# Optimization experiments

Measured on AMD Instinct MI355X. Metric: run time of the kernel, lower is better.

## Reference

```python
import jax, jax.numpy as jnp
import numpy as np

D_MODEL = 2048
N_HEADS = 32
N_KV_HEADS = 8
HEAD_DIM = D_MODEL // N_HEADS  # 64
ROPE_THETA = 10000.0


def _build_rope_cache(seq_len, head_dim, theta):
    half = head_dim // 2
    inv_freq = 1.0 / theta ** (jnp.arange(half, dtype=jnp.float32) / half)
    pos = jnp.arange(seq_len, dtype=jnp.float32)
    freqs = jnp.outer(pos, inv_freq)  # [S, half]
    return jnp.cos(freqs), jnp.sin(freqs)


def _apply_rope(x, cos, sin):
    # x: [B, H, S, D]; cos/sin: [S, D//2] -> broadcast [1,1,S,D//2]
    x_even = x[..., ::2]
    x_odd = x[..., 1::2]
    c = cos[None, None]
    s = sin[None, None]
    rot_even = x_even * c - x_odd * s
    rot_odd = x_even * s + x_odd * c
    # interleave back: stack on last axis then flatten
    return jnp.stack((rot_even, rot_odd), axis=-1).reshape(x.shape)


def setup_inputs() -> dict:
    key = jax.random.key(0)
    k0, k1, k2, k3, k4 = jax.random.split(key, 5)
    B, S = 2, 2048
    scale = 0.02
    x = jax.random.normal(k0, (B, S, D_MODEL), dtype=jnp.float32)
    Wq = jax.random.normal(k1, (D_MODEL, N_HEADS * HEAD_DIM), dtype=jnp.float32) * scale
    Wk = jax.random.normal(k2, (D_MODEL, N_KV_HEADS * HEAD_DIM), dtype=jnp.float32) * scale
    Wv = jax.random.normal(k3, (D_MODEL, N_KV_HEADS * HEAD_DIM), dtype=jnp.float32) * scale
    Wo = jax.random.normal(k4, (D_MODEL, D_MODEL), dtype=jnp.float32) * scale
    return {"x": x, "Wq": Wq, "Wk": Wk, "Wv": Wv, "Wo": Wo}


def reference(x, Wq, Wk, Wv, Wo):
    B, S, _ = x.shape
    q = (x @ Wq).reshape(B, S, N_HEADS, HEAD_DIM).transpose(0, 2, 1, 3)      # [B,H,S,D]
    k = (x @ Wk).reshape(B, S, N_KV_HEADS, HEAD_DIM).transpose(0, 2, 1, 3)   # [B,Hk,S,D]
    v = (x @ Wv).reshape(B, S, N_KV_HEADS, HEAD_DIM).transpose(0, 2, 1, 3)
    cos, sin = _build_rope_cache(S, HEAD_DIM, ROPE_THETA)
    q = _apply_rope(q, cos, sin)
    k = _apply_rope(k, cos, sin)
    repeat = N_HEADS // N_KV_HEADS
    if repeat > 1:
        k = jnp.repeat(k, repeat, axis=1)
        v = jnp.repeat(v, repeat, axis=1)
    scores = jnp.einsum("bhqd,bhkd->bhqk", q, k) / jnp.sqrt(jnp.float32(HEAD_DIM))
    causal = jnp.tril(jnp.ones((S, S), dtype=bool))
    neg = -jnp.finfo(scores.dtype).max
    scores = jnp.where(causal[None, None], scores, neg)
    probs = jax.nn.softmax(scores.astype(jnp.float32), axis=-1).astype(x.dtype)
    out = jnp.einsum("bhqk,bhkd->bhqd", probs, v)
    out = out.transpose(0, 2, 1, 3).reshape(B, S, D_MODEL)
    return out @ Wo
```

## Files before the change

kernel.cpp:

```cpp
#include <hip/hip_runtime.h>
#include <cstdint>

typedef unsigned short u16;
typedef __attribute__((ext_vector_type(8))) __bf16 bf16x8;
typedef __attribute__((ext_vector_type(4))) float f32x4;

#define S_LEN 2048

__device__ __forceinline__ u16 f2bf(float f) {
  uint32_t u = __builtin_bit_cast(uint32_t, f);
  u += 0x7fffu + ((u >> 16) & 1u);
  return (u16)(u >> 16);
}
__device__ __forceinline__ float bf2f(u16 h) {
  return __builtin_bit_cast(float, (uint32_t)h << 16);
}
__device__ __forceinline__ bf16x8 ldfrag(const u16* p) {
  return __builtin_bit_cast(bf16x8, *(const uint4*)p);
}
__device__ __forceinline__ f32x4 mfma16(bf16x8 a, bf16x8 b, f32x4 c) {
  return __builtin_amdgcn_mfma_f32_16x16x32_bf16(a, b, c, 0, 0, 0);
}
__device__ __forceinline__ void glds16(const u16* g, u16* l) {
  __builtin_amdgcn_global_load_lds((const __attribute__((address_space(1))) void*)g,
                                   (__attribute__((address_space(3))) void*)l, 16, 0, 0);
}

__global__ __launch_bounds__(256) void cvt_kernel(const float* __restrict__ in,
                                                  u16* __restrict__ out, int n4) {
  int i = blockIdx.x * 256 + threadIdx.x;
  if (i >= n4) return;
  float4 v = ((const float4*)in)[i];
  ushort4 o;
  o.x = f2bf(v.x); o.y = f2bf(v.y); o.z = f2bf(v.z); o.w = f2bf(v.w);
  ((ushort4*)out)[i] = o;
}

__global__ __launch_bounds__(256) void cvtT_kernel(const float* __restrict__ W,
                                                   u16* __restrict__ Wt, int K, int N) {
  __shared__ float t[32][33];
  int tx = threadIdx.x & 31, ty = threadIdx.x >> 5;
  int n0 = blockIdx.x * 32, k0 = blockIdx.y * 32;
#pragma unroll
  for (int j = 0; j < 4; ++j)
    t[ty + 8 * j][tx] = W[(long)(k0 + ty + 8 * j) * N + n0 + tx];
  __syncthreads();
#pragma unroll
  for (int j = 0; j < 4; ++j)
    Wt[(long)(n0 + ty + 8 * j) * K + k0 + tx] = f2bf(t[tx][ty + 8 * j]);
}

template <int MODE>
__global__ __launch_bounds__(256) void gemm_bt(const u16* __restrict__ A,
                                               const u16* __restrict__ Bt,
                                               void* __restrict__ C, int K, int ldc,
                                               u16* __restrict__ Kc_out,
                                               u16* __restrict__ Vt_out) {
  __shared__ __align__(16) u16 As[3][4096];
  __shared__ __align__(16) u16 Bs[3][4096];
  int tid = threadIdx.x;
  int lane = tid & 63, w = tid >> 6;
  int wr = (w >> 1) * 64, wc = (w & 1) * 64;
  int l15 = lane & 15, l4 = lane >> 4;
  int rowbase = blockIdx.x * 128, colbase = blockIdx.y * 128;
  f32x4 acc[4][4] = {};
  int r0 = tid >> 2, kc0 = (tid & 3) * 8;
  const u16* Ap0 = A + (long)(rowbase + r0) * K + kc0;
  const u16* Ap1 = A + (long)(rowbase + 64 + r0) * K + kc0;
  const u16* Bp0 = Bt + (long)(colbase + r0) * K + kc0;
  const u16* Bp1 = Bt + (long)(colbase + 64 + r0) * K + kc0;
  int wb = w * 512;
  auto stage = [&](int t, int buf) {
    int ko = t * 32;
    glds16(Ap0 + ko, &As[buf][wb]);
    glds16(Ap1 + ko, &As[buf][2048 + wb]);
    glds16(Bp0 + ko, &Bs[buf][wb]);
    glds16(Bp1 + ko, &Bs[buf][2048 + wb]);
  };
  int nk = K >> 5;
  stage(0, 0);
  stage(1, 1);
  asm volatile("s_waitcnt vmcnt(4)" ::: "memory");
  __builtin_amdgcn_s_barrier();
  int cur = 0, nxt2 = 2;
  for (int t = 0; t < nk; ++t) {
    if (t + 2 < nk) stage(t + 2, nxt2);
    bf16x8 af[4], bv[4];
#pragma unroll
    for (int m = 0; m < 4; ++m) af[m] = ldfrag(&As[cur][(wr + m * 16 + l15) * 32 + l4 * 8]);
#pragma unroll
    for (int n = 0; n < 4; ++n) bv[n] = ldfrag(&Bs[cur][(wc + n * 16 + l15) * 32 + l4 * 8]);
#pragma unroll
    for (int m = 0; m < 4; ++m)
#pragma unroll
      for (int n = 0; n < 4; ++n) acc[m][n] = mfma16(af[m], bv[n], acc[m][n]);
    if (t + 1 < nk) {
      if (t + 2 < nk)
        asm volatile("s_waitcnt vmcnt(4)" ::: "memory");
      else
        asm volatile("s_waitcnt vmcnt(0)" ::: "memory");
      __builtin_amdgcn_s_barrier();
    }
    cur = cur == 2 ? 0 : cur + 1;
    nxt2 = nxt2 == 2 ? 0 : nxt2 + 1;
  }
  if (MODE == 0) {
#pragma unroll
    for (int m = 0; m < 4; ++m)
#pragma unroll
      for (int n = 0; n < 4; ++n)
#pragma unroll
        for (int r = 0; r < 4; ++r) {
          int row = rowbase + wr + m * 16 + l4 * 4 + r;
          int col = colbase + wc + n * 16 + l15;
          ((float*)C)[(long)row * ldc + col] = acc[m][n][r];
        }
  } else {
    if (colbase < 2048) {
#pragma unroll
      for (int m = 0; m < 4; ++m)
#pragma unroll
        for (int n = 0; n < 4; ++n)
#pragma unroll
          for (int r = 0; r < 4; ++r) {
            int row = rowbase + wr + m * 16 + l4 * 4 + r;
            int col = colbase + wc + n * 16 + l15;
            ((u16*)C)[(long)row * 2048 + col] = f2bf(acc[m][n][r]);
          }
    } else if (colbase < 2560) {
#pragma unroll
      for (int m = 0; m < 4; ++m)
#pragma unroll
        for (int n = 0; n < 4; ++n)
#pragma unroll
          for (int r = 0; r < 4; ++r) {
            int row = rowbase + wr + m * 16 + l4 * 4 + r;
            int col = colbase + wc + n * 16 + l15 - 2048;
            Kc_out[(long)row * 512 + col] = f2bf(acc[m][n][r]);
          }
    } else {
#pragma unroll
      for (int m = 0; m < 4; ++m)
#pragma unroll
        for (int n = 0; n < 4; ++n) {
          int row = rowbase + wr + m * 16 + l4 * 4;
          int col = colbase + wc + n * 16 + l15 - 2560;
          int b_ = row >> 11, s_ = row & 2047;
          int kvh_ = col >> 6, d_ = col & 63;
          ushort4 pk;
          pk.x = f2bf(acc[m][n][0]); pk.y = f2bf(acc[m][n][1]);
          pk.z = f2bf(acc[m][n][2]); pk.w = f2bf(acc[m][n][3]);
          *(ushort4*)&Vt_out[((long)((b_ * 8 + kvh_) * 64 + d_)) * 2048 + s_] = pk;
        }
    }
  }
}

__global__ __launch_bounds__(256) void rope_tab_kernel(float2* __restrict__ ctab) {
  int idx = blockIdx.x * 256 + threadIdx.x;
  int i = idx & 31, s = idx >> 5;
  float freq = exp2f(-(float)i * (13.287712379549449f / 32.0f));
  float sn, cs;
  sincosf((float)s * freq, &sn, &cs);
  ctab[idx] = make_float2(cs, sn);
}

__global__ __launch_bounds__(256) void kpack_kernel(const u16* __restrict__ Ks,
                                                    const float2* __restrict__ ctab,
                                                    u16* __restrict__ Kp) {
  int idx = blockIdx.x * 256 + threadIdx.x;
  int lane = idx & 63, half = (idx >> 6) & 1, n = (idx >> 7) & 3;
  int t = (idx >> 9) & 31, kvh = (idx >> 14) & 7, b = idx >> 17;
  int l15 = lane & 15, l4 = lane >> 4;
  int s = t * 64 + n * 16 + l15;
  int d0 = half * 32 + l4 * 8;
  const u16* src = Ks + ((long)(b * 2048 + s)) * 512 + kvh * 64 + d0;
  uint4 v = *(const uint4*)src;
  const float2* ct = ctab + s * 32 + (d0 >> 1);
  uint32_t o[4];
#pragma unroll
  for (int jj = 0; jj < 4; ++jj) {
    uint32_t vw = ((const uint32_t*)&v)[jj];
    float2 cs = ct[jj];
    float e = bf2f((u16)vw), od = bf2f((u16)(vw >> 16));
    float re = e * cs.x - od * cs.y;
    float ro = e * cs.y + od * cs.x;
    o[jj] = (uint32_t)f2bf(re) | ((uint32_t)f2bf(ro) << 16);
  }
  *(uint4*)(Kp + (long)idx * 8) = *(uint4*)o;
}

__global__ __launch_bounds__(256) void vpack_kernel(const u16* __restrict__ Vt,
                                                    u16* __restrict__ Vp) {
  int idx = blockIdx.x * 256 + threadIdx.x;
  int lane = idx & 63, half = (idx >> 6) & 1, f = (idx >> 7) & 3;
  int t = (idx >> 9) & 31, kvh = (idx >> 14) & 7, b = idx >> 17;
  int l15 = lane & 15, l4 = lane >> 4;
  const u16* src = Vt + ((long)((b * 8 + kvh) * 64 + f * 16 + l15)) * 2048 +
                   t * 64 + half * 32 + l4 * 8;
  *(uint4*)(Vp + (long)idx * 8) = *(const uint4*)src;
}

__global__ __launch_bounds__(256, 8) void attn_kernel(const u16* __restrict__ Q,
                                                      const u16* __restrict__ Kp,
                                                      const u16* __restrict__ Vp,
                                                      const float2* __restrict__ ctab,
                                                      u16* __restrict__ O) {
  int bid = blockIdx.x;
  int p = bid & 31, h = (bid >> 5) & 31, b = bid >> 10;
  int kvh = h >> 2;
  int tid = threadIdx.x, lane = tid & 63, w = tid >> 6;
  int l15 = lane & 15, l4 = lane >> 4;
  int cc = (w + p) & 3;
  int c = cc == 0 ? 2 * p : cc == 1 ? 2 * p + 1 : cc == 2 ? 127 - 2 * p : 126 - 2 * p;
  int qb = c * 16;
  int nt = (c >> 2) + 1;
  __shared__ u16 Ps[4][16][72];
  u16(*myPs)[72] = Ps[w];
  const u16* Qh = Q + (long)b * S_LEN * 2048 + h * 64;
  const u16* Kh = Kp + (long)(b * 8 + kvh) * 131072;
  const u16* Vh = Vp + (long)(b * 8 + kvh) * 131072;
  u16* Oh = O + (long)b * S_LEN * 2048 + h * 64;
  int s = qb + l15;
  const u16* qp = Qh + (long)s * 2048;
  uint4 r0 = *(const uint4*)(qp + l4 * 8);
  uint4 r1 = *(const uint4*)(qp + 32 + l4 * 8);
  const float2* ct = ctab + (long)s * 32 + l4 * 4;
  uint32_t q0w[4], q1w[4];
#pragma unroll
  for (int jj = 0; jj < 4; ++jj) {
    float2 cs0 = ct[jj], cs1 = ct[16 + jj];
    uint32_t v0 = ((const uint32_t*)&r0)[jj], v1 = ((const uint32_t*)&r1)[jj];
    float e0 = bf2f((u16)v0), o0 = bf2f((u16)(v0 >> 16));
    float e1 = bf2f((u16)v1), o1 = bf2f((u16)(v1 >> 16));
    float a0 = (e0 * cs0.x - o0 * cs0.y) * 0.125f;
    float b0 = (e0 * cs0.y + o0 * cs0.x) * 0.125f;
    float a1 = (e1 * cs1.x - o1 * cs1.y) * 0.125f;
    float b1 = (e1 * cs1.y + o1 * cs1.x) * 0.125f;
    q0w[jj] = (uint32_t)f2bf(a0) | ((uint32_t)f2bf(b0) << 16);
    q1w[jj] = (uint32_t)f2bf(a1) | ((uint32_t)f2bf(b1) << 16);
  }
  bf16x8 qf0 = __builtin_bit_cast(bf16x8, *(uint4*)q0w);
  bf16x8 qf1 = __builtin_bit_cast(bf16x8, *(uint4*)q1w);
  float m_r = -INFINITY, l_r = 0.f;
  f32x4 oaccT[4] = {};
  int lane8 = lane * 8;
  for (int t = 0; t < nt; ++t) {
    const u16* kt = Kh + t * 4096;
    f32x4 sacc[4] = {};
#pragma unroll
    for (int n = 0; n < 4; ++n) {
      sacc[n] = mfma16(ldfrag(kt + n * 1024 + lane8), qf0, sacc[n]);
      sacc[n] = mfma16(ldfrag(kt + n * 1024 + 512 + lane8), qf1, sacc[n]);
    }
    if (t == nt - 1) {
      int kb = t * 64;
#pragma unroll
      for (int n = 0; n < 4; ++n) {
        int kc_ = kb + n * 16 + l4 * 4;
#pragma unroll
        for (int r = 0; r < 4; ++r)
          if (kc_ + r > qb + l15) sacc[n][r] = -1e30f;
      }
    }
    float mx = fmaxf(fmaxf(fmaxf(sacc[0][0], sacc[0][1]), fmaxf(sacc[0][2], sacc[0][3])),
                     fmaxf(fmaxf(sacc[1][0], sacc[1][1]), fmaxf(sacc[1][2], sacc[1][3])));
    mx = fmaxf(mx, fmaxf(fmaxf(fmaxf(sacc[2][0], sacc[2][1]), fmaxf(sacc[2][2], sacc[2][3])),
                         fmaxf(fmaxf(sacc[3][0], sacc[3][1]), fmaxf(sacc[3][2], sacc[3][3]))));
    mx = fmaxf(mx, __shfl_xor(mx, 16));
    mx = fmaxf(mx, __shfl_xor(mx, 32));
    float mn = fmaxf(m_r, mx);
    float fac = __expf(m_r - mn);
    m_r = mn;
    float rs = 0.f;
#pragma unroll
    for (int n = 0; n < 4; ++n) {
      float p0 = __expf(sacc[n][0] - mn);
      float p1 = __expf(sacc[n][1] - mn);
      float p2 = __expf(sacc[n][2] - mn);
      float p3 = __expf(sacc[n][3] - mn);
      rs += (p0 + p1) + (p2 + p3);
      ushort4 pk;
      pk.x = f2bf(p0); pk.y = f2bf(p1); pk.z = f2bf(p2); pk.w = f2bf(p3);
      *(ushort4*)&myPs[l15][n * 16 + l4 * 4] = pk;
    }
    rs += __shfl_xor(rs, 16);
    rs += __shfl_xor(rs, 32);
    l_r = l_r * fac + rs;
#pragma unroll
    for (int f = 0; f < 4; ++f) {
      oaccT[f][0] *= fac; oaccT[f][1] *= fac;
      oaccT[f][2] *= fac; oaccT[f][3] *= fac;
    }
    bf16x8 pa0 = ldfrag(&myPs[l15][l4 * 8]);
    bf16x8 pa1 = ldfrag(&myPs[l15][32 + l4 * 8]);
    const u16* vt = Vh + t * 4096;
#pragma unroll
    for (int f = 0; f < 4; ++f) {
      oaccT[f] = mfma16(ldfrag(vt + f * 1024 + lane8), pa0, oaccT[f]);
      oaccT[f] = mfma16(ldfrag(vt + f * 1024 + 512 + lane8), pa1, oaccT[f]);
    }
  }
  float linv = 1.f / l_r;
#pragma unroll
  for (int f = 0; f < 4; ++f) {
    ushort4 pk;
    pk.x = f2bf(oaccT[f][0] * linv); pk.y = f2bf(oaccT[f][1] * linv);
    pk.z = f2bf(oaccT[f][2] * linv); pk.w = f2bf(oaccT[f][3] * linv);
    *(ushort4*)&Oh[(long)(qb + l15) * 2048 + f * 16 + l4 * 4] = pk;
  }
}

extern "C" void kernel_launch(void* const* d_in, const int* in_sizes, int n_in,
                              void* d_out, int out_size, void* d_ws, size_t ws_size,
                              hipStream_t stream) {
  const float* x = (const float*)d_in[0];
  const float* Wq = (const float*)d_in[1];
  const float* Wk = (const float*)d_in[2];
  const float* Wv = (const float*)d_in[3];
  const float* Wo = (const float*)d_in[4];
  float* out = (float*)d_out;
  char* ws = (char*)d_ws;
  u16* xb = (u16*)(ws + 0);
  u16* WqkvT = (u16*)(ws + 16777216);
  u16* WoT = (u16*)(ws + 29360128);
  u16* Qs = (u16*)(ws + 37748736);
  u16* Ks = (u16*)(ws + 54525952);
  u16* Vt = (u16*)(ws + 58720256);
  u16* Os = (u16*)(ws + 62914560);
  u16* Kp = (u16*)(ws + 0);
  u16* Vp = (u16*)(ws + 4194304);
  float2* ctab = (float2*)(ws + 79691776);

  cvt_kernel<<<8192, 256, 0, stream>>>(x, xb, 2097152);
  cvtT_kernel<<<dim3(64, 64), 256, 0, stream>>>(Wq, WqkvT, 2048, 2048);
  cvtT_kernel<<<dim3(16, 64), 256, 0, stream>>>(Wk, WqkvT + 4194304, 2048, 512);
  cvtT_kernel<<<dim3(16, 64), 256, 0, stream>>>(Wv, WqkvT + 5242880, 2048, 512);
  cvtT_kernel<<<dim3(64, 64), 256, 0, stream>>>(Wo, WoT, 2048, 2048);
  rope_tab_kernel<<<256, 256, 0, stream>>>(ctab);
  gemm_bt<3><<<dim3(32, 24), 256, 0, stream>>>(xb, WqkvT, Qs, 2048, 2048, Ks, Vt);
  kpack_kernel<<<1024, 256, 0, stream>>>(Ks, ctab, Kp);
  vpack_kernel<<<1024, 256, 0, stream>>>(Vt, Vp);
  attn_kernel<<<2048, 256, 0, stream>>>(Qs, Kp, Vp, ctab, Os);
  gemm_bt<0><<<dim3(32, 16), 256, 0, stream>>>(Os, WoT, out, 2048, 2048, nullptr, nullptr);
}
```

Baseline: 369.3 us.

## Merge prep and pack launches, use exp2 softmax, hardware bf16 cvt, setprio

Merges the six conversion/rope-table launches into one prep kernel and the K/V pack kernels into one, cutting launch overhead and gaps between kernels. The f32-to-bf16 conversion now uses the hardware cast. Softmax switches to exp2 with log2(e) folded into the Q scale. MFMA sections are wrapped in s_setprio, and attention query-block assignment changes from a balanced interleave to a simple linear mapping. The simpler mapping may worsen load balance across causal blocks.

```diff
diff --git a/kernel.cpp b/kernel.cpp
--- a/kernel.cpp
+++ b/kernel.cpp
@@ -8,9 +8,11 @@
 #define S_LEN 2048
 
 __device__ __forceinline__ u16 f2bf(float f) {
-  uint32_t u = __builtin_bit_cast(uint32_t, f);
-  u += 0x7fffu + ((u >> 16) & 1u);
-  return (u16)(u >> 16);
+  __bf16 h = (__bf16)f;
+  return __builtin_bit_cast(u16, h);
+}
+__device__ __forceinline__ uint32_t pk2(float a, float b) {
+  return (uint32_t)f2bf(a) | ((uint32_t)f2bf(b) << 16);
 }
 __device__ __forceinline__ float bf2f(u16 h) {
   return __builtin_bit_cast(float, (uint32_t)h << 16);
@@ -26,21 +28,10 @@
                                    (__attribute__((address_space(3))) void*)l, 16, 0, 0);
 }
 
-__global__ __launch_bounds__(256) void cvt_kernel(const float* __restrict__ in,
-                                                  u16* __restrict__ out, int n4) {
-  int i = blockIdx.x * 256 + threadIdx.x;
-  if (i >= n4) return;
-  float4 v = ((const float4*)in)[i];
-  ushort4 o;
-  o.x = f2bf(v.x); o.y = f2bf(v.y); o.z = f2bf(v.z); o.w = f2bf(v.w);
-  ((ushort4*)out)[i] = o;
-}
-
-__global__ __launch_bounds__(256) void cvtT_kernel(const float* __restrict__ W,
-                                                   u16* __restrict__ Wt, int K, int N) {
-  __shared__ float t[32][33];
-  int tx = threadIdx.x & 31, ty = threadIdx.x >> 5;
-  int n0 = blockIdx.x * 32, k0 = blockIdx.y * 32;
+__device__ __forceinline__ void cvtT_body(const float* __restrict__ W, u16* __restrict__ Wt,
+                                          int K, int N, int n0, int k0, int tid,
+                                          float (*t)[33]) {
+  int tx = tid & 31, ty = tid >> 5;
 #pragma unroll
   for (int j = 0; j < 4; ++j)
     t[ty + 8 * j][tx] = W[(long)(k0 + ty + 8 * j) * N + n0 + tx];
@@ -48,6 +39,46 @@
 #pragma unroll
   for (int j = 0; j < 4; ++j)
     Wt[(long)(n0 + ty + 8 * j) * K + k0 + tx] = f2bf(t[tx][ty + 8 * j]);
+}
+
+__global__ __launch_bounds__(256) void prep_kernel(const float* __restrict__ x,
+                                                   const float* __restrict__ Wq,
+                                                   const float* __restrict__ Wk,
+                                                   const float* __restrict__ Wv,
+                                                   const float* __restrict__ Wo,
+                                                   u16* __restrict__ xb,
+                                                   u16* __restrict__ WqkvT,
+                                                   u16* __restrict__ WoT,
+                                                   float2* __restrict__ ctab) {
+  __shared__ float t[32][33];
+  int blk = blockIdx.x, tid = threadIdx.x;
+  if (blk < 8192) {
+    int i = blk * 256 + tid;
+    float4 v = ((const float4*)x)[i];
+    uint2 o;
+    o.x = pk2(v.x, v.y);
+    o.y = pk2(v.z, v.w);
+    ((uint2*)xb)[i] = o;
+  } else if (blk < 12288) {
+    int b2 = blk - 8192;
+    cvtT_body(Wq, WqkvT, 2048, 2048, (b2 & 63) * 32, (b2 >> 6) * 32, tid, t);
+  } else if (blk < 13312) {
+    int b2 = blk - 12288;
+    cvtT_body(Wk, WqkvT + 4194304, 2048, 512, (b2 & 15) * 32, (b2 >> 4) * 32, tid, t);
+  } else if (blk < 14336) {
+    int b2 = blk - 13312;
+    cvtT_body(Wv, WqkvT + 5242880, 2048, 512, (b2 & 15) * 32, (b2 >> 4) * 32, tid, t);
+  } else if (blk < 18432) {
+    int b2 = blk - 14336;
+    cvtT_body(Wo, WoT, 2048, 2048, (b2 & 63) * 32, (b2 >> 6) * 32, tid, t);
+  } else {
+    int idx = (blk - 18432) * 256 + tid;
+    int i = idx & 31, s = idx >> 5;
+    float freq = exp2f(-(float)i * (13.287712379549449f / 32.0f));
+    float sn, cs;
+    sincosf((float)s * freq, &sn, &cs);
+    ctab[idx] = make_float2(cs, sn);
+  }
 }
 
 template <int MODE>
@@ -147,58 +178,49 @@
           int col = colbase + wc + n * 16 + l15 - 2560;
           int b_ = row >> 11, s_ = row & 2047;
           int kvh_ = col >> 6, d_ = col & 63;
-          ushort4 pk;
-          pk.x = f2bf(acc[m][n][0]); pk.y = f2bf(acc[m][n][1]);
-          pk.z = f2bf(acc[m][n][2]); pk.w = f2bf(acc[m][n][3]);
-          *(ushort4*)&Vt_out[((long)((b_ * 8 + kvh_) * 64 + d_)) * 2048 + s_] = pk;
+          uint2 o2;
+          o2.x = pk2(acc[m][n][0], acc[m][n][1]);
+          o2.y = pk2(acc[m][n][2], acc[m][n][3]);
+          *(uint2*)&Vt_out[((long)((b_ * 8 + kvh_) * 64 + d_)) * 2048 + s_] = o2;
         }
     }
   }
 }
 
-__global__ __launch_bounds__(256) void rope_tab_kernel(float2* __restrict__ ctab) {
-  int idx = blockIdx.x * 256 + threadIdx.x;
-  int i = idx & 31, s = idx >> 5;
-  float freq = exp2f(-(float)i * (13.287712379549449f / 32.0f));
-  float sn, cs;
-  sincosf((float)s * freq, &sn, &cs);
-  ctab[idx] = make_float2(cs, sn);
-}
-
-__global__ __launch_bounds__(256) void kpack_kernel(const u16* __restrict__ Ks,
-                                                    const float2* __restrict__ ctab,
-                                                    u16* __restrict__ Kp) {
-  int idx = blockIdx.x * 256 + threadIdx.x;
-  int lane = idx & 63, half = (idx >> 6) & 1, n = (idx >> 7) & 3;
-  int t = (idx >> 9) & 31, kvh = (idx >> 14) & 7, b = idx >> 17;
-  int l15 = lane & 15, l4 = lane >> 4;
-  int s = t * 64 + n * 16 + l15;
-  int d0 = half * 32 + l4 * 8;
-  const u16* src = Ks + ((long)(b * 2048 + s)) * 512 + kvh * 64 + d0;
-  uint4 v = *(const uint4*)src;
-  const float2* ct = ctab + s * 32 + (d0 >> 1);
-  uint32_t o[4];
-#pragma unroll
-  for (int jj = 0; jj < 4; ++jj) {
-    uint32_t vw = ((const uint32_t*)&v)[jj];
-    float2 cs = ct[jj];
-    float e = bf2f((u16)vw), od = bf2f((u16)(vw >> 16));
-    float re = e * cs.x - od * cs.y;
-    float ro = e * cs.y + od * cs.x;
-    o[jj] = (uint32_t)f2bf(re) | ((uint32_t)f2bf(ro) << 16);
-  }
-  *(uint4*)(Kp + (long)idx * 8) = *(uint4*)o;
-}
-
-__global__ __launch_bounds__(256) void vpack_kernel(const u16* __restrict__ Vt,
-                                                    u16* __restrict__ Vp) {
-  int idx = blockIdx.x * 256 + threadIdx.x;
-  int lane = idx & 63, half = (idx >> 6) & 1, f = (idx >> 7) & 3;
-  int t = (idx >> 9) & 31, kvh = (idx >> 14) & 7, b = idx >> 17;
-  int l15 = lane & 15, l4 = lane >> 4;
-  const u16* src = Vt + ((long)((b * 8 + kvh) * 64 + f * 16 + l15)) * 2048 +
-                   t * 64 + half * 32 + l4 * 8;
-  *(uint4*)(Vp + (long)idx * 8) = *(const uint4*)src;
+__global__ __launch_bounds__(256) void kvpack_kernel(const u16* __restrict__ Ks,
+                                                     const float2* __restrict__ ctab,
+                                                     u16* __restrict__ Kp,
+                                                     const u16* __restrict__ Vt,
+                                                     u16* __restrict__ Vp) {
+  int blk = blockIdx.x;
+  if (blk < 1024) {
+    int idx = blk * 256 + threadIdx.x;
+    int lane = idx & 63, half = (idx >> 6) & 1, n = (idx >> 7) & 3;
+    int t = (idx >> 9) & 31, kvh = (idx >> 14) & 7, b = idx >> 17;
+    int l15 = lane & 15, l4 = lane >> 4;
+    int s = t * 64 + n * 16 + l15;
+    int d0 = half * 32 + l4 * 8;
+    const u16* src = Ks + ((long)(b * 2048 + s)) * 512 + kvh * 64 + d0;
+    uint4 v = *(const uint4*)src;
+    const float2* ct = ctab + s * 32 + (d0 >> 1);
+    uint32_t o[4];
+#pragma unroll
+    for (int jj = 0; jj < 4; ++jj) {
+      uint32_t vw = ((const uint32_t*)&v)[jj];
+      float2 cs = ct[jj];
+      float e = bf2f((u16)vw), od = bf2f((u16)(vw >> 16));
+      o[jj] = pk2(e * cs.x - od * cs.y, e * cs.y + od * cs.x);
+    }
+    *(uint4*)(Kp + (long)idx * 8) = *(uint4*)o;
+  } else {
+    int idx = (blk - 1024) * 256 + threadIdx.x;
+    int lane = idx & 63, half = (idx >> 6) & 1, f = (idx >> 7) & 3;
+    int t = (idx >> 9) & 31, kvh = (idx >> 14) & 7, b = idx >> 17;
+    int l15 = lane & 15, l4 = lane >> 4;
+    const u16* src = Vt + ((long)((b * 8 + kvh) * 64 + f * 16 + l15)) * 2048 +
+                     t * 64 + half * 32 + l4 * 8;
+    *(uint4*)(Vp + (long)idx * 8) = *(const uint4*)src;
+  }
 }
 
 __global__ __launch_bounds__(256, 8) void attn_kernel(const u16* __restrict__ Q,
@@ -207,14 +229,13 @@
                                                       const float2* __restrict__ ctab,
                                                       u16* __restrict__ O) {
   int bid = blockIdx.x;
-  int p = bid & 31, h = (bid >> 5) & 31, b = bid >> 10;
+  int i = bid & 31, h = (bid >> 5) & 31, b = bid >> 10;
   int kvh = h >> 2;
   int tid = threadIdx.x, lane = tid & 63, w = tid >> 6;
   int l15 = lane & 15, l4 = lane >> 4;
-  int cc = (w + p) & 3;
-  int c = cc == 0 ? 2 * p : cc == 1 ? 2 * p + 1 : cc == 2 ? 127 - 2 * p : 126 - 2 * p;
+  int c = 4 * i + w;
   int qb = c * 16;
-  int nt = (c >> 2) + 1;
+  int nt = i + 1;
   __shared__ u16 Ps[4][16][72];
   u16(*myPs)[72] = Ps[w];
   const u16* Qh = Q + (long)b * S_LEN * 2048 + h * 64;
@@ -226,6 +247,7 @@
   uint4 r0 = *(const uint4*)(qp + l4 * 8);
   uint4 r1 = *(const uint4*)(qp + 32 + l4 * 8);
   const float2* ct = ctab + (long)s * 32 + l4 * 4;
+  const float QSC = 0.18033688011112042f;
   uint32_t q0w[4], q1w[4];
 #pragma unroll
   for (int jj = 0; jj < 4; ++jj) {
@@ -233,12 +255,8 @@
     uint32_t v0 = ((const uint32_t*)&r0)[jj], v1 = ((const uint32_t*)&r1)[jj];
     float e0 = bf2f((u16)v0), o0 = bf2f((u16)(v0 >> 16));
     float e1 = bf2f((u16)v1), o1 = bf2f((u16)(v1 >> 16));
-    float a0 = (e0 * cs0.x - o0 * cs0.y) * 0.125f;
-    float b0 = (e0 * cs0.y + o0 * cs0.x) * 0.125f;
-    float a1 = (e1 * cs1.x - o1 * cs1.y) * 0.125f;
-    float b1 = (e1 * cs1.y + o1 * cs1.x) * 0.125f;
-    q0w[jj] = (uint32_t)f2bf(a0) | ((uint32_t)f2bf(b0) << 16);
-    q1w[jj] = (uint32_t)f2bf(a1) | ((uint32_t)f2bf(b1) << 16);
+    q0w[jj] = pk2((e0 * cs0.x - o0 * cs0.y) * QSC, (e0 * cs0.y + o0 * cs0.x) * QSC);
+    q1w[jj] = pk2((e1 * cs1.x - o1 * cs1.y) * QSC, (e1 * cs1.y + o1 * cs1.x) * QSC);
   }
   bf16x8 qf0 = __builtin_bit_cast(bf16x8, *(uint4*)q0w);
   bf16x8 qf1 = __builtin_bit_cast(bf16x8, *(uint4*)q1w);
@@ -248,11 +266,13 @@
   for (int t = 0; t < nt; ++t) {
     const u16* kt = Kh + t * 4096;
     f32x4 sacc[4] = {};
+    __builtin_amdgcn_s_setprio(1);
 #pragma unroll
     for (int n = 0; n < 4; ++n) {
       sacc[n] = mfma16(ldfrag(kt + n * 1024 + lane8), qf0, sacc[n]);
       sacc[n] = mfma16(ldfrag(kt + n * 1024 + 512 + lane8), qf1, sacc[n]);
     }
+    __builtin_amdgcn_s_setprio(0);
     if (t == nt - 1) {
       int kb = t * 64;
 #pragma unroll
@@ -270,19 +290,20 @@
     mx = fmaxf(mx, __shfl_xor(mx, 16));
     mx = fmaxf(mx, __shfl_xor(mx, 32));
     float mn = fmaxf(m_r, mx);
-    float fac = __expf(m_r - mn);
+    float fac = exp2f(m_r - mn);
     m_r = mn;
     float rs = 0.f;
 #pragma unroll
     for (int n = 0; n < 4; ++n) {
-      float p0 = __expf(sacc[n][0] - mn);
-      float p1 = __expf(sacc[n][1] - mn);
-      float p2 = __expf(sacc[n][2] - mn);
-      float p3 = __expf(sacc[n][3] - mn);
+      float p0 = exp2f(sacc[n][0] - mn);
+      float p1 = exp2f(sacc[n][1] - mn);
+      float p2 = exp2f(sacc[n][2] - mn);
+      float p3 = exp2f(sacc[n][3] - mn);
       rs += (p0 + p1) + (p2 + p3);
-      ushort4 pk;
-      pk.x = f2bf(p0); pk.y = f2bf(p1); pk.z = f2bf(p2); pk.w = f2bf(p3);
-      *(ushort4*)&myPs[l15][n * 16 + l4 * 4] = pk;
+      uint2 o2;
+      o2.x = pk2(p0, p1);
+      o2.y = pk2(p2, p3);
+      *(uint2*)&myPs[l15][n * 16 + l4 * 4] = o2;
     }
     rs += __shfl_xor(rs, 16);
     rs += __shfl_xor(rs, 32);
@@ -295,19 +316,21 @@
     bf16x8 pa0 = ldfrag(&myPs[l15][l4 * 8]);
     bf16x8 pa1 = ldfrag(&myPs[l15][32 + l4 * 8]);
     const u16* vt = Vh + t * 4096;
+    __builtin_amdgcn_s_setprio(1);
 #pragma unroll
     for (int f = 0; f < 4; ++f) {
       oaccT[f] = mfma16(ldfrag(vt + f * 1024 + lane8), pa0, oaccT[f]);
       oaccT[f] = mfma16(ldfrag(vt + f * 1024 + 512 + lane8), pa1, oaccT[f]);
     }
+    __builtin_amdgcn_s_setprio(0);
   }
   float linv = 1.f / l_r;
 #pragma unroll
   for (int f = 0; f < 4; ++f) {
-    ushort4 pk;
-    pk.x = f2bf(oaccT[f][0] * linv); pk.y = f2bf(oaccT[f][1] * linv);
-    pk.z = f2bf(oaccT[f][2] * linv); pk.w = f2bf(oaccT[f][3] * linv);
-    *(ushort4*)&Oh[(long)(qb + l15) * 2048 + f * 16 + l4 * 4] = pk;
+    uint2 o2;
+    o2.x = pk2(oaccT[f][0] * linv, oaccT[f][1] * linv);
+    o2.y = pk2(oaccT[f][2] * linv, oaccT[f][3] * linv);
+    *(uint2*)&Oh[(long)(qb + l15) * 2048 + f * 16 + l4 * 4] = o2;
   }
 }
 
@@ -332,15 +355,9 @@
   u16* Vp = (u16*)(ws + 4194304);
   float2* ctab = (float2*)(ws + 79691776);
 
-  cvt_kernel<<<8192, 256, 0, stream>>>(x, xb, 2097152);
-  cvtT_kernel<<<dim3(64, 64), 256, 0, stream>>>(Wq, WqkvT, 2048, 2048);
-  cvtT_kernel<<<dim3(16, 64), 256, 0, stream>>>(Wk, WqkvT + 4194304, 2048, 512);
-  cvtT_kernel<<<dim3(16, 64), 256, 0, stream>>>(Wv, WqkvT + 5242880, 2048, 512);
-  cvtT_kernel<<<dim3(64, 64), 256, 0, stream>>>(Wo, WoT, 2048, 2048);
-  rope_tab_kernel<<<256, 256, 0, stream>>>(ctab);
+  prep_kernel<<<18688, 256, 0, stream>>>(x, Wq, Wk, Wv, Wo, xb, WqkvT, WoT, ctab);
   gemm_bt<3><<<dim3(32, 24), 256, 0, stream>>>(xb, WqkvT, Qs, 2048, 2048, Ks, Vt);
-  kpack_kernel<<<1024, 256, 0, stream>>>(Ks, ctab, Kp);
-  vpack_kernel<<<1024, 256, 0, stream>>>(Vt, Vp);
+  kvpack_kernel<<<2048, 256, 0, stream>>>(Ks, ctab, Kp, Vt, Vp);
   attn_kernel<<<2048, 256, 0, stream>>>(Qs, Kp, Vp, ctab, Os);
   gemm_bt<0><<<dim3(32, 16), 256, 0, stream>>>(Os, WoT, out, 2048, 2048, nullptr, nullptr);
 }
```

Result: slower. 378.8 us (+2.6%).
